# Optimization experiments

Hardware: AMD Instinct MI355X
Metric: run time of the kernel (lower is better)

The kernel has to match this reference:

```python
import jax, jax.numpy as jnp
import numpy as np

N_HEAD = 16
MEMORY = 256  # band width: key j visible to query i iff i-MEMORY <= j <= i


def setup_inputs() -> dict:
    key = jax.random.key(0)
    k1, k2, k3 = jax.random.split(key, 3)
    B, T, C = 2, 2048, 1024
    x = jax.random.normal(k1, (B, T, C), dtype=jnp.float32)
    # Linear weights stored in x @ W layout (equivalent to torch Linear with W^T)
    W_attn = jax.random.normal(k2, (C, 3 * C), dtype=jnp.float32) * (1.0 / np.sqrt(C))
    W_proj = jax.random.normal(k3, (C, C), dtype=jnp.float32) * (1.0 / np.sqrt(C))
    return {"x": x, "W_attn": W_attn, "W_proj": W_proj}


def reference(x, W_attn, W_proj):
    B, T, C = x.shape
    H = N_HEAD
    D = C // H
    qkv = x @ W_attn                                   # [B,T,3C]
    q, k, v = jnp.split(qkv, 3, axis=-1)
    # [B,T,C] -> [B,H,T,D]
    q = q.reshape(B, T, H, D).transpose(0, 2, 1, 3)
    k = k.reshape(B, T, H, D).transpose(0, 2, 1, 3)
    v = v.reshape(B, T, H, D).transpose(0, 2, 1, 3)
    scale = 1.0 / np.sqrt(D)
    scores = jnp.einsum('bhqd,bhkd->bhqk', q, k) * scale
    # banded causal mask: j <= i and j >= i - MEMORY
    i = jnp.arange(T)[:, None]
    j = jnp.arange(T)[None, :]
    mask = (j <= i) & (j >= i - MEMORY)                # [T,T] bool
    scores = jnp.where(mask[None, None], scores, -jnp.inf)
    att = jax.nn.softmax(scores, axis=-1)              # each row has >=1 valid entry
    y = jnp.einsum('bhqk,bhkd->bhqd', att, v)          # [B,H,T,D]
    y = y.transpose(0, 2, 1, 3).reshape(B, T, C)
    return y @ W_proj
```

## Files before the change

kernel.cpp:

```cpp
#include <hip/hip_runtime.h>

typedef __bf16 bf16;
typedef __bf16 bf16x4 __attribute__((ext_vector_type(4)));
typedef __bf16 bf16x8 __attribute__((ext_vector_type(8)));
typedef float f32x4 __attribute__((ext_vector_type(4)));

#define T_SEQ 2048
#define CDIM  1024
#define QKV_LD 3072
#define MEM   256

#define GLOAD_LDS16(gp, lp) __builtin_amdgcn_global_load_lds( \
    (const __attribute__((address_space(1))) unsigned int*)(gp), \
    (__attribute__((address_space(3))) unsigned int*)(lp), 16, 0, 0)

#define BAR() do { __builtin_amdgcn_s_barrier(); asm volatile("" ::: "memory"); } while (0)

__global__ __launch_bounds__(256) void prep_kernel(const float* __restrict__ x,
                                                   const float* __restrict__ Wa,
                                                   const float* __restrict__ Wp,
                                                   bf16* __restrict__ xb,
                                                   bf16* __restrict__ WaT,
                                                   bf16* __restrict__ WpT) {
    const int bid = blockIdx.x;
    if (bid < 4096) {
        int i = bid * 256 + threadIdx.x;
        float4 v = reinterpret_cast<const float4*>(x)[i];
        bf16x4 o = { (bf16)v.x, (bf16)v.y, (bf16)v.z, (bf16)v.w };
        reinterpret_cast<bf16x4*>(xb)[i] = o;
        return;
    }
    const float* W; bf16* Wt; int N, bx, by;
    if (bid < 4864) { W = Wa; Wt = WaT; N = 3072; int idx = bid - 4096; bx = idx % 48; by = idx / 48; }
    else            { W = Wp; Wt = WpT; N = 1024; int idx = bid - 4864; bx = idx % 16; by = idx / 16; }
    __shared__ float tile[64][65];
    const int n0 = bx * 64;
    const int k0 = by * 64;
    const int t  = threadIdx.x;
    const int tr = t >> 4;
    const int tc = (t & 15) * 4;
#pragma unroll
    for (int it = 0; it < 4; ++it) {
        int r = it * 16 + tr;
        float4 v = *reinterpret_cast<const float4*>(&W[(size_t)(k0 + r) * N + n0 + tc]);
        tile[r][tc + 0] = v.x; tile[r][tc + 1] = v.y;
        tile[r][tc + 2] = v.z; tile[r][tc + 3] = v.w;
    }
    __syncthreads();
#pragma unroll
    for (int it = 0; it < 4; ++it) {
        int n = it * 16 + tr;
        bf16x4 o;
#pragma unroll
        for (int j = 0; j < 4; ++j) o[j] = (bf16)tile[tc + j][n];
        *reinterpret_cast<bf16x4*>(&Wt[(size_t)(n0 + n) * 1024 + k0 + tc]) = o;
    }
}

__global__ __launch_bounds__(512, 4) void gemm256_kernel(const bf16* __restrict__ A,
                                                         const bf16* __restrict__ Bt,
                                                         bf16* __restrict__ Cb,
                                                         bf16* __restrict__ Vt,
                                                         int M, int N, int K) {
    __shared__ bf16 smA[2][128][64];
    __shared__ bf16 smB[2][192][64];
    const int t    = threadIdx.x;
    const int lane = t & 63;
    const int w    = t >> 6;
    const int wm   = (w >> 2) * 64;
    const int wn   = (w & 3) * 48;
    const int g    = lane >> 4;
    const int r    = lane & 15;

    const int nwg = gridDim.x, cpx = nwg >> 3;
    const int swz = (blockIdx.x & 7) * cpx + (blockIdx.x >> 3);
    const int ntn = N / 192;
    const int m0 = (swz / ntn) * 128;
    const int n0 = (swz % ntn) * 192;

    const bf16* Ab = A  + (size_t)m0 * K;
    const bf16* Bb = Bt + (size_t)n0 * K;
    const int NT = K >> 6;

#define STAGE_A(bi, u, kt) do { \
        const bf16* _s = Ab + (size_t)((u) * 64 + w * 8 + (lane >> 3)) * K \
                         + (kt) * 64 + ((lane & 7) ^ (lane >> 3)) * 8; \
        GLOAD_LDS16(_s, &smA[bi][(u) * 64 + w * 8][0]); \
    } while (0)
#define STAGE_B(bi, u, kt) do { \
        const bf16* _s = Bb + (size_t)((u) * 64 + w * 8 + (lane >> 3)) * K \
                         + (kt) * 64 + ((lane & 7) ^ (lane >> 3)) * 8; \
        GLOAD_LDS16(_s, &smB[bi][(u) * 64 + w * 8][0]); \
    } while (0)

    const int ch0 = ((g     ) ^ (r & 7)) * 8;
    const int ch1 = ((g ^ 4) ^ (r & 7)) * 8;

    const f32x4 zero4 = {0.f, 0.f, 0.f, 0.f};
    f32x4 acc[4][3];
#pragma unroll
    for (int i = 0; i < 4; ++i)
#pragma unroll
        for (int j = 0; j < 3; ++j) acc[i][j] = zero4;

    bf16x8 afr[4][2], bfrA[2][2], bfrB[1][2];

#define MGRP(BF, FNB, NF) do { \
    __builtin_amdgcn_s_setprio(1); \
    _Pragma("unroll") \
    for (int fm2 = 0; fm2 < 4; ++fm2) \
    _Pragma("unroll") \
    for (int fn2 = 0; fn2 < (NF); ++fn2) \
    _Pragma("unroll") \
    for (int kh = 0; kh < 2; ++kh) \
        acc[fm2][(FNB)+fn2] = __builtin_amdgcn_mfma_f32_16x16x32_bf16( \
            afr[fm2][kh], BF[fn2][kh], acc[fm2][(FNB)+fn2], 0, 0, 0); \
    __builtin_amdgcn_s_setprio(0); } while (0)

    STAGE_A(0, 0, 0); STAGE_A(0, 1, 0);
    STAGE_B(0, 0, 0); STAGE_B(0, 1, 0); STAGE_B(0, 2, 0);
    STAGE_A(1, 0, 1); STAGE_A(1, 1, 1);
    asm volatile("s_waitcnt vmcnt(2)" ::: "memory");
    __builtin_amdgcn_sched_barrier(0);
    BAR();

    for (int kt = 0; kt < NT; ++kt) {
        const int cur = kt & 1, nxt = cur ^ 1;
#pragma unroll
        for (int i = 0; i < 4; ++i) {
            afr[i][0] = *reinterpret_cast<const bf16x8*>(&smA[cur][wm + i * 16 + r][ch0]);
            afr[i][1] = *reinterpret_cast<const bf16x8*>(&smA[cur][wm + i * 16 + r][ch1]);
        }
#pragma unroll
        for (int fn = 0; fn < 2; ++fn) {
            bfrA[fn][0] = *reinterpret_cast<const bf16x8*>(&smB[cur][wn + fn * 16 + r][ch0]);
            bfrA[fn][1] = *reinterpret_cast<const bf16x8*>(&smB[cur][wn + fn * 16 + r][ch1]);
        }
        bfrB[0][0] = *reinterpret_cast<const bf16x8*>(&smB[cur][wn + 32 + r][ch0]);
        bfrB[0][1] = *reinterpret_cast<const bf16x8*>(&smB[cur][wn + 32 + r][ch1]);
        if (kt + 1 < NT) { STAGE_B(nxt, 0, kt + 1); STAGE_B(nxt, 1, kt + 1); STAGE_B(nxt, 2, kt + 1); }
        __builtin_amdgcn_sched_barrier(0);
        BAR();

        MGRP(bfrA, 0, 2);
        if (kt + 2 < NT) STAGE_A(cur, 0, kt + 2);
        MGRP(bfrB, 2, 1);
        if (kt + 2 < NT) STAGE_A(cur, 1, kt + 2);

        if (kt >= NT - 2)      { asm volatile("s_waitcnt vmcnt(0)" ::: "memory"); }
        else                   { asm volatile("s_waitcnt vmcnt(2)" ::: "memory"); }
        __builtin_amdgcn_sched_barrier(0);
        BAR();
    }

#pragma unroll
    for (int fm = 0; fm < 4; ++fm)
#pragma unroll
        for (int fn = 0; fn < 3; ++fn) {
            const int col  = n0 + wn + fn * 16 + r;
            const int row0 = m0 + wm + fm * 16 + g * 4;
            if (col < 2 * CDIM) {
#pragma unroll
                for (int e = 0; e < 4; ++e)
                    Cb[(size_t)(row0 + e) * N + col] = (bf16)acc[fm][fn][e];
            } else {
                const int hd = col - 2 * CDIM;
                const int bb = row0 >> 11, tt = row0 & (T_SEQ - 1);
                bf16x4 v = { (bf16)acc[fm][fn][0], (bf16)acc[fm][fn][1],
                             (bf16)acc[fm][fn][2], (bf16)acc[fm][fn][3] };
                *reinterpret_cast<bf16x4*>(&Vt[((size_t)(bb * 16 + (hd >> 6)) * 64 + (hd & 63)) * T_SEQ + tt]) = v;
            }
        }
#undef STAGE_A
#undef STAGE_B
#undef MGRP
}

__global__ __launch_bounds__(256) void proj_kernel(const bf16* __restrict__ A,
                                                   const bf16* __restrict__ Bt,
                                                   float* __restrict__ Cf,
                                                   int M, int N, int K) {
    __shared__ bf16 As[128 * 32];
    __shared__ bf16 Bs[64 * 32];
    const int t    = threadIdx.x;
    const int lane = t & 63;
    const int w    = t >> 6;
    const int wm   = (w >> 1) * 64;
    const int wn   = (w & 1) * 32;
    const int g    = lane >> 4;
    const int r    = lane & 15;
    const int m0   = blockIdx.y * 128;
    const int n0   = blockIdx.x * 64;

    const bf16* Ab = A  + (size_t)m0 * K;
    const bf16* Bb = Bt + (size_t)n0 * K;
    const bf16* Ag0 = Ab + (size_t)(w * 32 + (lane >> 2)) * K + (lane & 3) * 8;
    const bf16* Ag1 = Ab + (size_t)(w * 32 + 16 + (lane >> 2)) * K + (lane & 3) * 8;
    const bf16* Bg0 = Bb + (size_t)(w * 16 + (lane >> 2)) * K + (lane & 3) * 8;

    bf16* ldsA0 = As + (w * 32) * 32;
    bf16* ldsA1 = As + (w * 32 + 16) * 32;
    bf16* ldsB0 = Bs + (w * 16) * 32;

    const f32x4 zero4 = {0.f, 0.f, 0.f, 0.f};
    f32x4 acc[4][2];
#pragma unroll
    for (int i = 0; i < 4; ++i)
#pragma unroll
        for (int j = 0; j < 2; ++j) acc[i][j] = zero4;

    for (int k0 = 0; k0 < K; k0 += 32) {
        __syncthreads();
        GLOAD_LDS16(Ag0 + k0, ldsA0);
        GLOAD_LDS16(Ag1 + k0, ldsA1);
        GLOAD_LDS16(Bg0 + k0, ldsB0);
        __syncthreads();

        bf16x8 af[4], bfr[2];
#pragma unroll
        for (int i = 0; i < 4; ++i)
            af[i]  = *reinterpret_cast<const bf16x8*>(&As[(wm + i * 16 + r) * 32 + g * 8]);
#pragma unroll
        for (int j = 0; j < 2; ++j)
            bfr[j] = *reinterpret_cast<const bf16x8*>(&Bs[(wn + j * 16 + r) * 32 + g * 8]);
#pragma unroll
        for (int i = 0; i < 4; ++i)
#pragma unroll
            for (int j = 0; j < 2; ++j)
                acc[i][j] = __builtin_amdgcn_mfma_f32_16x16x32_bf16(af[i], bfr[j], acc[i][j], 0, 0, 0);
    }

#pragma unroll
    for (int i = 0; i < 4; ++i)
#pragma unroll
        for (int j = 0; j < 2; ++j)
#pragma unroll
            for (int e = 0; e < 4; ++e) {
                int row = m0 + wm + i * 16 + g * 4 + e;
                int col = n0 + wn + j * 16 + r;
                Cf[(size_t)row * N + col] = acc[i][j][e];
            }
}

__global__ __launch_bounds__(512) void attn_kernel(const bf16* __restrict__ qkv,
                                                   const bf16* __restrict__ Vt,
                                                   bf16* __restrict__ y) {
    __shared__ bf16 vtl[64 * 384];
    const int bid  = blockIdx.x;
    const int bh   = bid >> 4;
    const int qblk = bid & 15;
    const int b = bh >> 4, h = bh & 15;
    const int qb0 = qblk * 128;
    const int wlo = qb0 - 256;
    const int wv   = threadIdx.x >> 6;
    const int lane = threadIdx.x & 63;
    const int g = lane >> 4, c = lane & 15;
    const int q0 = qb0 + wv * 16;
    const int q = q0 + c;
    const float NEG_INF = -__builtin_inff();

    const bf16* base = qkv + (size_t)b * T_SEQ * QKV_LD;
    const bf16* Qb = base + h * 64;
    const bf16* Kb = base + CDIM + h * 64;
    const bf16* Vtb = Vt + (size_t)(b * 16 + h) * 64 * T_SEQ;

#pragma unroll
    for (int i = 0; i < 6; ++i) {
        const int Lb = (wv * 6 + i) * 1024 + lane * 16;
        const int d   = Lb / 768;
        const int c16 = (Lb % 768) >> 4;
        int koff = ((2 * c16) ^ (d & 14)) << 2;
        int gk = wlo + koff;
        gk = gk < 0 ? 0 : gk;
        GLOAD_LDS16(Vtb + (size_t)d * T_SEQ + gk, vtl + (wv * 6 + i) * 512);
    }

    const bf16x8 qf0 = *reinterpret_cast<const bf16x8*>(Qb + (size_t)q * QKV_LD + g * 8);
    const bf16x8 qf1 = *reinterpret_cast<const bf16x8*>(Qb + (size_t)q * QKV_LD + 32 + g * 8);

    __syncthreads();

    const f32x4 zero4 = {0.f, 0.f, 0.f, 0.f};
    f32x4 o[4];
#pragma unroll
    for (int cb = 0; cb < 4; ++cb) o[cb] = zero4;
    float m_run = NEG_INF, l_run = 0.f;

#define LOAD_K(J0, K00, K01, K10, K11) do { \
        const int _kr0 = (J0) + c; \
        int _kr1 = (J0) + 16 + c; _kr1 = _kr1 < T_SEQ ? _kr1 : T_SEQ - 1; \
        K00 = *reinterpret_cast<const bf16x8*>(Kb + (size_t)_kr0 * QKV_LD + g * 8); \
        K01 = *reinterpret_cast<const bf16x8*>(Kb + (size_t)_kr0 * QKV_LD + 32 + g * 8); \
        K10 = *reinterpret_cast<const bf16x8*>(Kb + (size_t)_kr1 * QKV_LD + g * 8); \
        K11 = *reinterpret_cast<const bf16x8*>(Kb + (size_t)_kr1 * QKV_LD + 32 + g * 8); \
    } while (0)

    const int jstart = (q0 - MEM > 0) ? (q0 - MEM) : 0;
    bf16x8 kc00, kc01, kc10, kc11;
    LOAD_K(jstart, kc00, kc01, kc10, kc11);

    for (int j0 = jstart; j0 < q0 + 16; j0 += 32) {
        bf16x8 kn00, kn01, kn10, kn11;
        const bool more = (j0 + 32 < q0 + 16);
        if (more) LOAD_K(j0 + 32, kn00, kn01, kn10, kn11);

        f32x4 s0 = __builtin_amdgcn_mfma_f32_16x16x32_bf16(kc00, qf0, zero4, 0, 0, 0);
        s0 = __builtin_amdgcn_mfma_f32_16x16x32_bf16(kc01, qf1, s0, 0, 0, 0);
        f32x4 s1 = __builtin_amdgcn_mfma_f32_16x16x32_bf16(kc10, qf0, zero4, 0, 0, 0);
        s1 = __builtin_amdgcn_mfma_f32_16x16x32_bf16(kc11, qf1, s1, 0, 0, 0);

        float mt = NEG_INF;
#pragma unroll
        for (int e = 0; e < 4; ++e) {
            int k0i = j0 + 4 * g + e;
            int k1i = k0i + 16;
            float v0 = (k0i <= q && k0i >= q - MEM) ? s0[e] * 0.125f : NEG_INF;
            float v1 = (k1i <= q && k1i >= q - MEM) ? s1[e] * 0.125f : NEG_INF;
            s0[e] = v0; s1[e] = v1;
            mt = fmaxf(mt, fmaxf(v0, v1));
        }
        mt = fmaxf(mt, __shfl_xor(mt, 16, 64));
        mt = fmaxf(mt, __shfl_xor(mt, 32, 64));
        const float mnew = fmaxf(m_run, mt);
        const float corr = __expf(m_run - mnew);

        float ps = 0.f;
        bf16x8 pav;
#pragma unroll
        for (int e = 0; e < 4; ++e) {
            float e0 = __expf(s0[e] - mnew);
            float e1 = __expf(s1[e] - mnew);
            ps += e0 + e1;
            pav[e]     = (bf16)e0;
            pav[4 + e] = (bf16)e1;
        }
        ps += __shfl_xor(ps, 16, 64);
        ps += __shfl_xor(ps, 32, 64);
        l_run = l_run * corr + ps;
        m_run = mnew;

#pragma unroll
        for (int cb = 0; cb < 4; ++cb) {
            o[cb][0] *= corr; o[cb][1] *= corr; o[cb][2] *= corr; o[cb][3] *= corr;
        }

        const int jrel = j0 - wlo;
        const int c8a = (jrel + 4 * g) >> 2;
        const int c8b = (c8a + 4 > 95) ? 95 : (c8a + 4);
#pragma unroll
        for (int cb = 0; cb < 4; ++cb) {
            const int d = cb * 16 + c;
            const int xx = d & 14;
            const bf16* vrow = vtl + d * 384;
            bf16x4 va  = *reinterpret_cast<const bf16x4*>(vrow + ((c8a ^ xx) << 2));
            bf16x4 vb2 = *reinterpret_cast<const bf16x4*>(vrow + ((c8b ^ xx) << 2));
            bf16x8 vf = { va[0], va[1], va[2], va[3], vb2[0], vb2[1], vb2[2], vb2[3] };
            o[cb] = __builtin_amdgcn_mfma_f32_16x16x32_bf16(vf, pav, o[cb], 0, 0, 0);
        }

        if (more) { kc00 = kn00; kc01 = kn01; kc10 = kn10; kc11 = kn11; }
    }
#undef LOAD_K

    const float linv = 1.0f / l_run;
    bf16* yr = y + (size_t)(b * T_SEQ + q) * CDIM + h * 64 + 4 * g;
#pragma unroll
    for (int cb = 0; cb < 4; ++cb) {
        bf16x4 ov = { (bf16)(o[cb][0] * linv), (bf16)(o[cb][1] * linv),
                      (bf16)(o[cb][2] * linv), (bf16)(o[cb][3] * linv) };
        *reinterpret_cast<bf16x4*>(yr + cb * 16) = ov;
    }
}

extern "C" void kernel_launch(void* const* d_in, const int* in_sizes, int n_in,
                              void* d_out, int out_size, void* d_ws, size_t ws_size,
                              hipStream_t stream) {
    const float* x      = (const float*)d_in[0];
    const float* W_attn = (const float*)d_in[1];
    const float* W_proj = (const float*)d_in[2];
    float* out = (float*)d_out;

    char* ws = (char*)d_ws;
    bf16* xb   = (bf16*)(ws);
    bf16* WaT  = (bf16*)(ws + 8388608);
    bf16* WpT  = (bf16*)(ws + 14680064);
    bf16* qkv  = (bf16*)(ws + 16777216);
    bf16* yatt = (bf16*)(ws + 41943040);
    bf16* Vt   = (bf16*)(ws + 50331648);

    prep_kernel<<<5120, 256, 0, stream>>>(x, W_attn, W_proj, xb, WaT, WpT);
    gemm256_kernel<<<512, 512, 0, stream>>>(xb, WaT, qkv, Vt, 4096, 3072, 1024);
    attn_kernel<<<512, 512, 0, stream>>>(qkv, Vt, yatt);
    proj_kernel<<<dim3(16, 32), 256, 0, stream>>>(yatt, WpT, out, 4096, 1024, 1024);
}
```

Before: 91.51 us.

## Widen attention key step to 64, add lazy rescale and interior mask skip

```diff
diff --git a/kernel.cpp b/kernel.cpp
--- a/kernel.cpp
+++ b/kernel.cpp
@@ -286,81 +286,93 @@
     for (int cb = 0; cb < 4; ++cb) o[cb] = zero4;
     float m_run = NEG_INF, l_run = 0.f;
 
-#define LOAD_K(J0, K00, K01, K10, K11) do { \
-        const int _kr0 = (J0) + c; \
-        int _kr1 = (J0) + 16 + c; _kr1 = _kr1 < T_SEQ ? _kr1 : T_SEQ - 1; \
-        K00 = *reinterpret_cast<const bf16x8*>(Kb + (size_t)_kr0 * QKV_LD + g * 8); \
-        K01 = *reinterpret_cast<const bf16x8*>(Kb + (size_t)_kr0 * QKV_LD + 32 + g * 8); \
-        K10 = *reinterpret_cast<const bf16x8*>(Kb + (size_t)_kr1 * QKV_LD + g * 8); \
-        K11 = *reinterpret_cast<const bf16x8*>(Kb + (size_t)_kr1 * QKV_LD + 32 + g * 8); \
-    } while (0)
-
     const int jstart = (q0 - MEM > 0) ? (q0 - MEM) : 0;
-    bf16x8 kc00, kc01, kc10, kc11;
-    LOAD_K(jstart, kc00, kc01, kc10, kc11);
-
-    for (int j0 = jstart; j0 < q0 + 16; j0 += 32) {
-        bf16x8 kn00, kn01, kn10, kn11;
-        const bool more = (j0 + 32 < q0 + 16);
-        if (more) LOAD_K(j0 + 32, kn00, kn01, kn10, kn11);
-
-        f32x4 s0 = __builtin_amdgcn_mfma_f32_16x16x32_bf16(kc00, qf0, zero4, 0, 0, 0);
-        s0 = __builtin_amdgcn_mfma_f32_16x16x32_bf16(kc01, qf1, s0, 0, 0, 0);
-        f32x4 s1 = __builtin_amdgcn_mfma_f32_16x16x32_bf16(kc10, qf0, zero4, 0, 0, 0);
-        s1 = __builtin_amdgcn_mfma_f32_16x16x32_bf16(kc11, qf1, s1, 0, 0, 0);
+    for (int j0 = jstart; j0 < q0 + 16; j0 += 64) {
+        bf16x8 kf[4][2];
+#pragma unroll
+        for (int su = 0; su < 4; ++su) {
+            int kr = j0 + 16 * su + c; kr = kr < T_SEQ ? kr : T_SEQ - 1;
+            kf[su][0] = *reinterpret_cast<const bf16x8*>(Kb + (size_t)kr * QKV_LD + g * 8);
+            kf[su][1] = *reinterpret_cast<const bf16x8*>(Kb + (size_t)kr * QKV_LD + 32 + g * 8);
+        }
+        f32x4 s[4];
+#pragma unroll
+        for (int su = 0; su < 4; ++su) {
+            s[su] = __builtin_amdgcn_mfma_f32_16x16x32_bf16(kf[su][0], qf0, zero4, 0, 0, 0);
+            s[su] = __builtin_amdgcn_mfma_f32_16x16x32_bf16(kf[su][1], qf1, s[su], 0, 0, 0);
+        }
 
         float mt = NEG_INF;
-#pragma unroll
-        for (int e = 0; e < 4; ++e) {
-            int k0i = j0 + 4 * g + e;
-            int k1i = k0i + 16;
-            float v0 = (k0i <= q && k0i >= q - MEM) ? s0[e] * 0.125f : NEG_INF;
-            float v1 = (k1i <= q && k1i >= q - MEM) ? s1[e] * 0.125f : NEG_INF;
-            s0[e] = v0; s1[e] = v1;
-            mt = fmaxf(mt, fmaxf(v0, v1));
+        const bool interior = (j0 + 63 <= q0) && (j0 >= q0 - 241);
+        if (interior) {
+#pragma unroll
+            for (int su = 0; su < 4; ++su)
+#pragma unroll
+                for (int e = 0; e < 4; ++e) {
+                    s[su][e] *= 0.125f;
+                    mt = fmaxf(mt, s[su][e]);
+                }
+        } else {
+#pragma unroll
+            for (int su = 0; su < 4; ++su)
+#pragma unroll
+                for (int e = 0; e < 4; ++e) {
+                    int ki = j0 + 16 * su + 4 * g + e;
+                    float v = (ki <= q && ki >= q - MEM) ? s[su][e] * 0.125f : NEG_INF;
+                    s[su][e] = v;
+                    mt = fmaxf(mt, v);
+                }
         }
         mt = fmaxf(mt, __shfl_xor(mt, 16, 64));
         mt = fmaxf(mt, __shfl_xor(mt, 32, 64));
-        const float mnew = fmaxf(m_run, mt);
-        const float corr = __expf(m_run - mnew);
+
+        if (!__all(mt <= m_run + 8.f)) {
+            const float mnew = fmaxf(m_run, mt);
+            const float corr = __expf(m_run - mnew);
+#pragma unroll
+            for (int cb = 0; cb < 4; ++cb) {
+                o[cb][0] *= corr; o[cb][1] *= corr; o[cb][2] *= corr; o[cb][3] *= corr;
+            }
+            l_run *= corr;
+            m_run = mnew;
+        }
 
         float ps = 0.f;
-        bf16x8 pav;
+        bf16x8 pav0, pav1;
 #pragma unroll
         for (int e = 0; e < 4; ++e) {
-            float e0 = __expf(s0[e] - mnew);
-            float e1 = __expf(s1[e] - mnew);
-            ps += e0 + e1;
-            pav[e]     = (bf16)e0;
-            pav[4 + e] = (bf16)e1;
+            float e0 = __expf(s[0][e] - m_run);
+            float e1 = __expf(s[1][e] - m_run);
+            float e2 = __expf(s[2][e] - m_run);
+            float e3 = __expf(s[3][e] - m_run);
+            ps += (e0 + e1) + (e2 + e3);
+            pav0[e] = (bf16)e0; pav0[4 + e] = (bf16)e1;
+            pav1[e] = (bf16)e2; pav1[4 + e] = (bf16)e3;
         }
         ps += __shfl_xor(ps, 16, 64);
         ps += __shfl_xor(ps, 32, 64);
-        l_run = l_run * corr + ps;
-        m_run = mnew;
-
-#pragma unroll
-        for (int cb = 0; cb < 4; ++cb) {
-            o[cb][0] *= corr; o[cb][1] *= corr; o[cb][2] *= corr; o[cb][3] *= corr;
-        }
+        l_run += ps;
 
         const int jrel = j0 - wlo;
-        const int c8a = (jrel + 4 * g) >> 2;
-        const int c8b = (c8a + 4 > 95) ? 95 : (c8a + 4);
+        const int c8 = (jrel + 4 * g) >> 2;
+        const int c8b1 = (c8 + 4  > 95) ? 95 : (c8 + 4);
+        const int c8b2 = (c8 + 8  > 95) ? 95 : (c8 + 8);
+        const int c8b3 = (c8 + 12 > 95) ? 95 : (c8 + 12);
 #pragma unroll
         for (int cb = 0; cb < 4; ++cb) {
             const int d = cb * 16 + c;
             const int xx = d & 14;
             const bf16* vrow = vtl + d * 384;
-            bf16x4 va  = *reinterpret_cast<const bf16x4*>(vrow + ((c8a ^ xx) << 2));
-            bf16x4 vb2 = *reinterpret_cast<const bf16x4*>(vrow + ((c8b ^ xx) << 2));
-            bf16x8 vf = { va[0], va[1], va[2], va[3], vb2[0], vb2[1], vb2[2], vb2[3] };
-            o[cb] = __builtin_amdgcn_mfma_f32_16x16x32_bf16(vf, pav, o[cb], 0, 0, 0);
-        }
-
-        if (more) { kc00 = kn00; kc01 = kn01; kc10 = kn10; kc11 = kn11; }
-    }
-#undef LOAD_K
+            bf16x4 v0 = *reinterpret_cast<const bf16x4*>(vrow + ((c8   ^ xx) << 2));
+            bf16x4 v1 = *reinterpret_cast<const bf16x4*>(vrow + ((c8b1 ^ xx) << 2));
+            bf16x4 v2 = *reinterpret_cast<const bf16x4*>(vrow + ((c8b2 ^ xx) << 2));
+            bf16x4 v3 = *reinterpret_cast<const bf16x4*>(vrow + ((c8b3 ^ xx) << 2));
+            bf16x8 vf0 = { v0[0], v0[1], v0[2], v0[3], v1[0], v1[1], v1[2], v1[3] };
+            bf16x8 vf1 = { v2[0], v2[1], v2[2], v2[3], v3[0], v3[1], v3[2], v3[3] };
+            o[cb] = __builtin_amdgcn_mfma_f32_16x16x32_bf16(vf0, pav0, o[cb], 0, 0, 0);
+            o[cb] = __builtin_amdgcn_mfma_f32_16x16x32_bf16(vf1, pav1, o[cb], 0, 0, 0);
+        }
+    }
 
     const float linv = 1.0f / l_run;
     bf16* yr = y + (size_t)(b * T_SEQ + q) * CDIM + h * 64 + 4 * g;
```

New measurement: 93.05 us. Within noise of the previous version (+1.7%).

## Restructure QKV GEMM pipeline, remap tiles per XCD, stage V transpose in LDS

Applied to the files above, without the earlier changes.

```diff
diff --git a/kernel.cpp b/kernel.cpp
--- a/kernel.cpp
+++ b/kernel.cpp
@@ -62,8 +62,9 @@
                                                          bf16* __restrict__ Cb,
                                                          bf16* __restrict__ Vt,
                                                          int M, int N, int K) {
-    __shared__ bf16 smA[2][128][64];
-    __shared__ bf16 smB[2][192][64];
+    __shared__ bf16 lds[40960];
+#define SMA(bi, row) (lds + (((bi) * 128 + (row)) << 6))
+#define SMB(bi, row) (lds + 16384 + (((bi) * 192 + (row)) << 6))
     const int t    = threadIdx.x;
     const int lane = t & 63;
     const int w    = t >> 6;
@@ -72,11 +73,12 @@
     const int g    = lane >> 4;
     const int r    = lane & 15;
 
-    const int nwg = gridDim.x, cpx = nwg >> 3;
-    const int swz = (blockIdx.x & 7) * cpx + (blockIdx.x >> 3);
-    const int ntn = N / 192;
-    const int m0 = (swz / ntn) * 128;
-    const int n0 = (swz % ntn) * 192;
+    const int xcd   = blockIdx.x & 7;
+    const int local = blockIdx.x >> 3;
+    const int mt = (xcd >> 1) * 8 + (local >> 3);
+    const int nt = (xcd & 1) * 8 + (local & 7);
+    const int m0 = mt * 128;
+    const int n0 = nt * 192;
 
     const bf16* Ab = A  + (size_t)m0 * K;
     const bf16* Bb = Bt + (size_t)n0 * K;
@@ -85,12 +87,12 @@
 #define STAGE_A(bi, u, kt) do { \
         const bf16* _s = Ab + (size_t)((u) * 64 + w * 8 + (lane >> 3)) * K \
                          + (kt) * 64 + ((lane & 7) ^ (lane >> 3)) * 8; \
-        GLOAD_LDS16(_s, &smA[bi][(u) * 64 + w * 8][0]); \
+        GLOAD_LDS16(_s, SMA(bi, (u) * 64 + w * 8)); \
     } while (0)
 #define STAGE_B(bi, u, kt) do { \
         const bf16* _s = Bb + (size_t)((u) * 64 + w * 8 + (lane >> 3)) * K \
                          + (kt) * 64 + ((lane & 7) ^ (lane >> 3)) * 8; \
-        GLOAD_LDS16(_s, &smB[bi][(u) * 64 + w * 8][0]); \
+        GLOAD_LDS16(_s, SMB(bi, (u) * 64 + w * 8)); \
     } while (0)
 
     const int ch0 = ((g     ) ^ (r & 7)) * 8;
@@ -119,8 +121,7 @@
 
     STAGE_A(0, 0, 0); STAGE_A(0, 1, 0);
     STAGE_B(0, 0, 0); STAGE_B(0, 1, 0); STAGE_B(0, 2, 0);
-    STAGE_A(1, 0, 1); STAGE_A(1, 1, 1);
-    asm volatile("s_waitcnt vmcnt(2)" ::: "memory");
+    asm volatile("s_waitcnt vmcnt(0)" ::: "memory");
     __builtin_amdgcn_sched_barrier(0);
     BAR();
 
@@ -128,31 +129,31 @@
         const int cur = kt & 1, nxt = cur ^ 1;
 #pragma unroll
         for (int i = 0; i < 4; ++i) {
-            afr[i][0] = *reinterpret_cast<const bf16x8*>(&smA[cur][wm + i * 16 + r][ch0]);
-            afr[i][1] = *reinterpret_cast<const bf16x8*>(&smA[cur][wm + i * 16 + r][ch1]);
+            afr[i][0] = *reinterpret_cast<const bf16x8*>(SMA(cur, wm + i * 16 + r) + ch0);
+            afr[i][1] = *reinterpret_cast<const bf16x8*>(SMA(cur, wm + i * 16 + r) + ch1);
         }
 #pragma unroll
         for (int fn = 0; fn < 2; ++fn) {
-            bfrA[fn][0] = *reinterpret_cast<const bf16x8*>(&smB[cur][wn + fn * 16 + r][ch0]);
-            bfrA[fn][1] = *reinterpret_cast<const bf16x8*>(&smB[cur][wn + fn * 16 + r][ch1]);
-        }
-        bfrB[0][0] = *reinterpret_cast<const bf16x8*>(&smB[cur][wn + 32 + r][ch0]);
-        bfrB[0][1] = *reinterpret_cast<const bf16x8*>(&smB[cur][wn + 32 + r][ch1]);
-        if (kt + 1 < NT) { STAGE_B(nxt, 0, kt + 1); STAGE_B(nxt, 1, kt + 1); STAGE_B(nxt, 2, kt + 1); }
+            bfrA[fn][0] = *reinterpret_cast<const bf16x8*>(SMB(cur, wn + fn * 16 + r) + ch0);
+            bfrA[fn][1] = *reinterpret_cast<const bf16x8*>(SMB(cur, wn + fn * 16 + r) + ch1);
+        }
+        bfrB[0][0] = *reinterpret_cast<const bf16x8*>(SMB(cur, wn + 32 + r) + ch0);
+        bfrB[0][1] = *reinterpret_cast<const bf16x8*>(SMB(cur, wn + 32 + r) + ch1);
+
+        if (kt + 1 < NT) {
+            STAGE_A(nxt, 0, kt + 1); STAGE_A(nxt, 1, kt + 1);
+            STAGE_B(nxt, 0, kt + 1); STAGE_B(nxt, 1, kt + 1); STAGE_B(nxt, 2, kt + 1);
+        }
+
+        MGRP(bfrA, 0, 2);
+        MGRP(bfrB, 2, 1);
+
+        asm volatile("s_waitcnt vmcnt(0)" ::: "memory");
         __builtin_amdgcn_sched_barrier(0);
         BAR();
-
-        MGRP(bfrA, 0, 2);
-        if (kt + 2 < NT) STAGE_A(cur, 0, kt + 2);
-        MGRP(bfrB, 2, 1);
-        if (kt + 2 < NT) STAGE_A(cur, 1, kt + 2);
-
-        if (kt >= NT - 2)      { asm volatile("s_waitcnt vmcnt(0)" ::: "memory"); }
-        else                   { asm volatile("s_waitcnt vmcnt(2)" ::: "memory"); }
-        __builtin_amdgcn_sched_barrier(0);
-        BAR();
-    }
-
+    }
+
+    bf16* stage = lds + (size_t)w * (48 * 72);
 #pragma unroll
     for (int fm = 0; fm < 4; ++fm)
 #pragma unroll
@@ -164,16 +165,30 @@
                 for (int e = 0; e < 4; ++e)
                     Cb[(size_t)(row0 + e) * N + col] = (bf16)acc[fm][fn][e];
             } else {
-                const int hd = col - 2 * CDIM;
-                const int bb = row0 >> 11, tt = row0 & (T_SEQ - 1);
-                bf16x4 v = { (bf16)acc[fm][fn][0], (bf16)acc[fm][fn][1],
-                             (bf16)acc[fm][fn][2], (bf16)acc[fm][fn][3] };
-                *reinterpret_cast<bf16x4*>(&Vt[((size_t)(bb * 16 + (hd >> 6)) * 64 + (hd & 63)) * T_SEQ + tt]) = v;
+                const int dl = fn * 16 + r;
+                const int tl = fm * 16 + g * 4;
+#pragma unroll
+                for (int e = 0; e < 4; ++e)
+                    stage[dl * 72 + tl + e] = (bf16)acc[fm][fn][e];
             }
         }
+    if (n0 + wn + 47 >= 2 * CDIM) {
+        if (lane < 48 && (n0 + wn + lane) >= 2 * CDIM) {
+            const int hd = n0 + wn + lane - 2 * CDIM;
+            const int bb = m0 >> 11;
+            const int tt = (m0 & (T_SEQ - 1)) + wm;
+            bf16* dst = &Vt[((size_t)(bb * 16 + (hd >> 6)) * 64 + (hd & 63)) * T_SEQ + tt];
+            const bf16* srcl = stage + lane * 72;
+#pragma unroll
+            for (int jj = 0; jj < 8; ++jj)
+                reinterpret_cast<bf16x8*>(dst)[jj] = reinterpret_cast<const bf16x8*>(srcl)[jj];
+        }
+    }
 #undef STAGE_A
 #undef STAGE_B
 #undef MGRP
+#undef SMA
+#undef SMB
 }
 
 __global__ __launch_bounds__(256) void proj_kernel(const bf16* __restrict__ A,
```

After: 91.12 us. About the same (-0.4%).
